# Performance work log

Measured on AMD Instinct MI355X. Metric: run time of the kernel, lower is better.

The kernel has to match this reference:

```python
import jax, jax.numpy as jnp
import numpy as np

N_NODES = 100000
N_EDGES = 1600000
N_GRAPHS = 2048
IN_C, HID, OUT_C, EDGE_DIM = 32, 128, 1, 3


def _glorot(key, shape):
    fan_in, fan_out = shape[0], shape[1]
    lim = np.sqrt(6.0 / (fan_in + fan_out))
    return jax.random.uniform(key, shape, jnp.float32, -lim, lim)


def setup_inputs() -> dict:
    key = jax.random.key(0)
    ks = jax.random.split(key, 16)
    x = jax.random.normal(ks[0], (N_NODES, IN_C), jnp.float32)
    edge_index = jax.random.randint(ks[1], (2, N_EDGES), 0, N_NODES, jnp.int64)
    edge_attr = jax.random.uniform(ks[2], (N_EDGES, EDGE_DIM), jnp.float32)
    batch = jnp.sort(jax.random.randint(ks[3], (N_NODES,), 0, N_GRAPHS, jnp.int64))
    params = {
        # GINEConv 1: edge lin 3->32, nn1: 32->128->128
        "We1": _glorot(ks[4], (EDGE_DIM, IN_C)), "be1": jnp.zeros((IN_C,), jnp.float32),
        "W1a": _glorot(ks[5], (IN_C, HID)), "b1a": jnp.zeros((HID,), jnp.float32),
        "W1b": _glorot(ks[6], (HID, HID)), "b1b": jnp.zeros((HID,), jnp.float32),
        # GINEConv 2: edge lin 3->128, nn2: 128->128->128
        "We2": _glorot(ks[7], (EDGE_DIM, HID)), "be2": jnp.zeros((HID,), jnp.float32),
        "W2a": _glorot(ks[8], (HID, HID)), "b2a": jnp.zeros((HID,), jnp.float32),
        "W2b": _glorot(ks[9], (HID, HID)), "b2b": jnp.zeros((HID,), jnp.float32),
        # readout MLP: 128->128->1
        "Wm1": _glorot(ks[10], (HID, HID)), "bm1": jnp.zeros((HID,), jnp.float32),
        "Wm2": _glorot(ks[11], (HID, OUT_C)), "bm2": jnp.zeros((OUT_C,), jnp.float32),
    }
    return {"x": x, "edge_index": edge_index, "edge_attr": edge_attr, "batch": batch, **params}


def _gine_conv(x, src, dst, edge_attr, We, be, Wa, ba, Wb, bb):
    # message: relu(x_j + lin(edge_attr)); aggregate: scatter-add at dst; eps=0
    msg = jax.nn.relu(x[src] + edge_attr @ We + be)          # [E, C]
    agg = jax.ops.segment_sum(msg, dst, num_segments=x.shape[0])
    h = x + agg                                              # (1+eps)*x + agg, eps=0
    return jax.nn.relu(h @ Wa + ba) @ Wb + bb


def reference(x, edge_index, edge_attr, batch,
              We1, be1, W1a, b1a, W1b, b1b,
              We2, be2, W2a, b2a, W2b, b2b,
              Wm1, bm1, Wm2, bm2):
    src, dst = edge_index[0], edge_index[1]
    h = jax.nn.relu(_gine_conv(x, src, dst, edge_attr, We1, be1, W1a, b1a, W1b, b1b))
    h = jax.nn.relu(_gine_conv(h, src, dst, edge_attr, We2, be2, W2a, b2a, W2b, b2b))
    pooled = jax.ops.segment_sum(h, batch, num_segments=N_GRAPHS)  # global_add_pool
    return jax.nn.relu(pooled @ Wm1 + bm1) @ Wm2 + bm2
```

## Files before the change

### kernel.cpp

```cpp
#include <hip/hip_runtime.h>
#include <hip/hip_bf16.h>

#define NN 100000
#define NE 1600000
#define NG 2048
#define NBKT 196
#define EPB 4096
#define BINBLKS ((NE + EPB - 1) / EPB)

typedef __attribute__((ext_vector_type(8))) short short8v;
typedef __attribute__((ext_vector_type(4))) float f32x4;

__device__ inline ushort f2bf(float f) {
    uint u = __float_as_uint(f);
    uint r = (u + 0x7fffu + ((u >> 16) & 1u)) >> 16;
    return (ushort)r;
}
__device__ inline float bf2f(ushort h) {
    return __uint_as_float(((uint)h) << 16);
}

#define MFMA_BF16 __builtin_amdgcn_mfma_f32_16x16x32_bf16

__device__ inline int frag128(int k, int c) {
    int w = c >> 5, half = (c >> 4) & 1, cl = c & 15;
    int ksl = k >> 5, kq = (k >> 3) & 3, k0 = k & 7;
    return ((ksl * 4 + w) * 2 + half) * 512 + (kq * 16 + cl) * 8 + k0;
}
__device__ inline int frag32(int k, int c) {
    int w = c >> 5, half = (c >> 4) & 1, cl = c & 15;
    int kq = (k >> 3) & 3, k0 = k & 7;
    return (w * 2 + half) * 512 + (kq * 16 + cl) * 8 + k0;
}


__global__ __launch_bounds__(256) void k_bhist(const int* __restrict__ dst,
                                               int* __restrict__ bhist) {
    __shared__ int h[NBKT];
    int t = threadIdx.x;
    for (int i = t; i < NBKT; i += 256) h[i] = 0;
    __syncthreads();
    int e0 = blockIdx.x * EPB;
    int n = NE - e0; if (n > EPB) n = EPB;
    for (int i = t; i < n; i += 256)
        atomicAdd(&h[dst[e0 + i] >> 9], 1);
    __syncthreads();
    for (int i = t; i < NBKT; i += 256)
        if (h[i]) atomicAdd(&bhist[i], h[i]);
}

__global__ void k_bscan(const int* __restrict__ bhist,
                        int* __restrict__ bkt_off, int* __restrict__ bkt_cursor) {
    __shared__ int s[256];
    int t = threadIdx.x;
    int v = (t < NBKT) ? bhist[t] : 0;
    s[t] = v;
    __syncthreads();
    for (int off = 1; off < 256; off <<= 1) {
        int add = (t >= off) ? s[t - off] : 0;
        __syncthreads();
        s[t] += add;
        __syncthreads();
    }
    int excl = s[t] - v;
    if (t < NBKT) { bkt_off[t] = excl; bkt_cursor[t] = excl; }
    if (t == NBKT - 1) bkt_off[NBKT] = excl + v;
}


__global__ __launch_bounds__(256) void k_binfill(
        const int* __restrict__ src, const int* __restrict__ dst,
        const float* __restrict__ ea,
        int* __restrict__ bkt_cursor, uint2* __restrict__ tmp) {
    __shared__ int hist[NBKT];
    __shared__ int boff[NBKT];
    __shared__ int base[NBKT];
    __shared__ int s[256];
    __shared__ uint2 stage[EPB];
    __shared__ unsigned char stage_bkt[EPB];
    int t = threadIdx.x;
    int e0 = blockIdx.x * EPB;
    int n = NE - e0; if (n > EPB) n = EPB;

    for (int i = t; i < NBKT; i += 256) hist[i] = 0;
    __syncthreads();

    uint lo[16], hi[16]; int bk[16], pos[16];
#pragma unroll
    for (int j = 0; j < 16; ++j) {
        int i = j * 256 + t;
        bk[j] = -1;
        if (i < n) {
            int e = e0 + i;
            int sn = src[e], d = dst[e];
            uint q0 = (uint)__float2int_rn(ea[3 * e]     * 1023.f);
            uint q1 = (uint)__float2int_rn(ea[3 * e + 1] * 1023.f);
            uint q2 = (uint)__float2int_rn(ea[3 * e + 2] * 1023.f);
            uint q = (q0 << 20) | (q1 << 10) | q2;
            lo[j] = (uint)sn | ((uint)(d & 0x7FFF) << 17);
            hi[j] = (uint)(d >> 15) | (q << 2);
            bk[j] = d >> 9;
            pos[j] = atomicAdd(&hist[bk[j]], 1);
        }
    }
    __syncthreads();
    int v = (t < NBKT) ? hist[t] : 0;
    s[t] = v;
    __syncthreads();
    for (int off = 1; off < 256; off <<= 1) {
        int add = (t >= off) ? s[t - off] : 0;
        __syncthreads();
        s[t] += add;
        __syncthreads();
    }
    if (t < NBKT) {
        boff[t] = s[t] - v;
        base[t] = v ? atomicAdd(&bkt_cursor[t], v) : 0;
    }
    __syncthreads();
#pragma unroll
    for (int j = 0; j < 16; ++j) {
        if (bk[j] >= 0) {
            int slot = boff[bk[j]] + pos[j];
            stage[slot] = make_uint2(lo[j], hi[j]);
            stage_bkt[slot] = (unsigned char)bk[j];
        }
    }
    __syncthreads();
    for (int i = t; i < n; i += 256) {
        int b = stage_bkt[i];
        tmp[base[b] + (i - boff[b])] = stage[i];
    }
}


__global__ __launch_bounds__(256) void k_scatter(
        const uint2* __restrict__ tmp, const int* __restrict__ bkt_off,
        int* __restrict__ row_ptr, uint2* __restrict__ csr) {
    __shared__ int hist[512];
    __shared__ int cur[512];
    __shared__ int s[256];
    int b = blockIdx.x, t = threadIdx.x;
    int start = bkt_off[b], end = bkt_off[b + 1];
    hist[t] = 0; hist[t + 256] = 0;
    __syncthreads();
    for (int i = start + t; i < end; i += 256) {
        uint2 r = tmp[i];
        int d = (int)((r.x >> 17) | ((r.y & 3u) << 15));
        atomicAdd(&hist[d & 511], 1);
    }
    __syncthreads();
    int h0 = hist[2 * t], h1 = hist[2 * t + 1];
    int v = h0 + h1;
    s[t] = v;
    __syncthreads();
    for (int off = 1; off < 256; off <<= 1) {
        int add = (t >= off) ? s[t - off] : 0;
        __syncthreads();
        s[t] += add;
        __syncthreads();
    }
    int e0 = start + s[t] - v;
    int node0 = b * 512 + 2 * t;
    if (node0 < NN) row_ptr[node0] = e0;
    if (node0 + 1 < NN) row_ptr[node0 + 1] = e0 + h0;
    cur[2 * t] = e0;
    cur[2 * t + 1] = e0 + h0;
    if (b == NBKT - 1 && t == 0) row_ptr[NN] = end;
    __syncthreads();
    for (int i = start + t; i < end; i += 256) {
        uint2 r = tmp[i];
        int sn = (int)(r.x & 0x1FFFFu);
        int d = (int)((r.x >> 17) | ((r.y & 3u) << 15));
        int p = atomicAdd(&cur[d & 511], 1);
        csr[p] = make_uint2((uint)sn, r.y >> 2);
    }
}


__global__ void k_xcast(const float* __restrict__ x, ushort* __restrict__ xb) {
    int i = blockIdx.x * 256 + threadIdx.x;
    if (i < NN * 32 / 4) {
        float4 v = ((const float4*)x)[i];
        ushort4 o;
        o.x = f2bf(v.x); o.y = f2bf(v.y); o.z = f2bf(v.z); o.w = f2bf(v.w);
        ((ushort4*)xb)[i] = o;
    }
}


__global__ void k_prep(const float* __restrict__ W1a, const float* __restrict__ W1b,
                       const float* __restrict__ W2a, const float* __restrict__ W2b,
                       ushort* __restrict__ W1a_hi, ushort* __restrict__ W1a_lo,
                       ushort* __restrict__ W1b_hi, ushort* __restrict__ W1b_lo,
                       ushort* __restrict__ W2a_hi, ushort* __restrict__ W2a_lo,
                       ushort* __restrict__ W2b_hi, ushort* __restrict__ W2b_lo) {
    int i = blockIdx.x * 256 + threadIdx.x;
    float v; ushort* ph; ushort* pl; int off;
    if (i < 4096) {
        int k = i >> 7, c = i & 127;
        v = W1a[i]; ph = W1a_hi; pl = W1a_lo; off = frag32(k, c);
    } else if (i < 20480) {
        int j = i - 4096; int k = j >> 7, c = j & 127;
        v = W1b[j]; ph = W1b_hi; pl = W1b_lo; off = frag128(k, c);
    } else if (i < 36864) {
        int j = i - 20480; int k = j >> 7, c = j & 127;
        v = W2a[j]; ph = W2a_hi; pl = W2a_lo; off = frag128(k, c);
    } else if (i < 53248) {
        int j = i - 36864; int k = j >> 7, c = j & 127;
        v = W2b[j]; ph = W2b_hi; pl = W2b_lo; off = frag128(k, c);
    } else return;
    ushort h = f2bf(v);
    ph[off] = h;
    pl[off] = f2bf(v - bf2f(h));
}


__global__ __launch_bounds__(256) void k_agg1(
        const ushort* __restrict__ xb, const uint2* __restrict__ csr,
        const int* __restrict__ row_ptr,
        const float* __restrict__ We1, const float* __restrict__ be1,
        float* __restrict__ agg1) {
    int lane = threadIdx.x & 31;
    int node = blockIdx.x * 8 + (threadIdx.x >> 5);
    const float qs = 1.f / 1023.f;
    float w0 = We1[lane] * qs, w1 = We1[32 + lane] * qs, w2 = We1[64 + lane] * qs;
    float b = be1[lane];
    int p0 = row_ptr[node], p1 = row_ptr[node + 1];
    float acc = 0.f;
    int p = p0;
    for (; p + 8 <= p1; p += 8) {
        uint2 e[8]; ushort v[8];
#pragma unroll
        for (int j = 0; j < 8; ++j) e[j] = csr[p + j];
#pragma unroll
        for (int j = 0; j < 8; ++j) v[j] = xb[e[j].x * 32 + lane];
#pragma unroll
        for (int j = 0; j < 8; ++j) {
            float a0 = (float)(e[j].y >> 20);
            float a1 = (float)((e[j].y >> 10) & 1023u);
            float a2 = (float)(e[j].y & 1023u);
            float el = fmaf(a0, w0, fmaf(a1, w1, fmaf(a2, w2, b)));
            acc += fmaxf(bf2f(v[j]) + el, 0.f);
        }
    }
    for (; p + 4 <= p1; p += 4) {
        uint2 e[4]; ushort v[4];
#pragma unroll
        for (int j = 0; j < 4; ++j) e[j] = csr[p + j];
#pragma unroll
        for (int j = 0; j < 4; ++j) v[j] = xb[e[j].x * 32 + lane];
#pragma unroll
        for (int j = 0; j < 4; ++j) {
            float a0 = (float)(e[j].y >> 20);
            float a1 = (float)((e[j].y >> 10) & 1023u);
            float a2 = (float)(e[j].y & 1023u);
            float el = fmaf(a0, w0, fmaf(a1, w1, fmaf(a2, w2, b)));
            acc += fmaxf(bf2f(v[j]) + el, 0.f);
        }
    }
    for (; p < p1; ++p) {
        uint2 ed = csr[p];
        ushort v = xb[ed.x * 32 + lane];
        float a0 = (float)(ed.y >> 20);
        float a1 = (float)((ed.y >> 10) & 1023u);
        float a2 = (float)(ed.y & 1023u);
        float el = fmaf(a0, w0, fmaf(a1, w1, fmaf(a2, w2, b)));
        acc += fmaxf(bf2f(v) + el, 0.f);
    }
    agg1[node * 32 + lane] = acc;
}


__global__ __launch_bounds__(256) void k_agg2(
        const ushort* __restrict__ h1b, const uint2* __restrict__ csr,
        const int* __restrict__ row_ptr,
        const float* __restrict__ We2, const float* __restrict__ be2,
        float* __restrict__ agg2) {
    int lane = threadIdx.x & 63;
    int node = __builtin_amdgcn_readfirstlane(blockIdx.x * 4 + (threadIdx.x >> 6));
    int c = lane * 2;
    const float qs = 1.f / 1023.f;
    float w0a = We2[c] * qs,       w0b = We2[c + 1] * qs;
    float w1a = We2[128 + c] * qs, w1b = We2[129 + c] * qs;
    float w2a = We2[256 + c] * qs, w2b = We2[257 + c] * qs;
    float ba  = be2[c],            bb  = be2[c + 1];
    const uint* h1u = (const uint*)h1b;
    int p0 = __builtin_amdgcn_readfirstlane(row_ptr[node]);
    int p1 = __builtin_amdgcn_readfirstlane(row_ptr[node + 1]);
    float accA = 0.f, accB = 0.f;
    int p = p0;
    for (; p + 8 <= p1; p += 8) {
        uint2 e[8]; uint u[8];
#pragma unroll
        for (int j = 0; j < 8; ++j) e[j] = csr[p + j];
#pragma unroll
        for (int j = 0; j < 8; ++j) u[j] = h1u[e[j].x * 64 + lane];
#pragma unroll
        for (int j = 0; j < 8; ++j) {
            float a0 = (float)(e[j].y >> 20);
            float a1 = (float)((e[j].y >> 10) & 1023u);
            float a2 = (float)(e[j].y & 1023u);
            float elA = fmaf(a0, w0a, fmaf(a1, w1a, fmaf(a2, w2a, ba)));
            float elB = fmaf(a0, w0b, fmaf(a1, w1b, fmaf(a2, w2b, bb)));
            accA += fmaxf(bf2f((ushort)(u[j] & 0xffffu)) + elA, 0.f);
            accB += fmaxf(bf2f((ushort)(u[j] >> 16)) + elB, 0.f);
        }
    }
    for (; p + 4 <= p1; p += 4) {
        uint2 e[4]; uint u[4];
#pragma unroll
        for (int j = 0; j < 4; ++j) e[j] = csr[p + j];
#pragma unroll
        for (int j = 0; j < 4; ++j) u[j] = h1u[e[j].x * 64 + lane];
#pragma unroll
        for (int j = 0; j < 4; ++j) {
            float a0 = (float)(e[j].y >> 20);
            float a1 = (float)((e[j].y >> 10) & 1023u);
            float a2 = (float)(e[j].y & 1023u);
            float elA = fmaf(a0, w0a, fmaf(a1, w1a, fmaf(a2, w2a, ba)));
            float elB = fmaf(a0, w0b, fmaf(a1, w1b, fmaf(a2, w2b, bb)));
            accA += fmaxf(bf2f((ushort)(u[j] & 0xffffu)) + elA, 0.f);
            accB += fmaxf(bf2f((ushort)(u[j] >> 16)) + elB, 0.f);
        }
    }
    for (; p < p1; ++p) {
        uint2 ed = csr[p];
        uint u = h1u[ed.x * 64 + lane];
        float a0 = (float)(ed.y >> 20);
        float a1 = (float)((ed.y >> 10) & 1023u);
        float a2 = (float)(ed.y & 1023u);
        float elA = fmaf(a0, w0a, fmaf(a1, w1a, fmaf(a2, w2a, ba)));
        float elB = fmaf(a0, w0b, fmaf(a1, w1b, fmaf(a2, w2b, bb)));
        accA += fmaxf(bf2f((ushort)(u & 0xffffu)) + elA, 0.f);
        accB += fmaxf(bf2f((ushort)(u >> 16)) + elB, 0.f);
    }
    *(float2*)&agg2[node * 128 + c] = make_float2(accA, accB);
}


#define M1_AHI 0
#define M1_ALO 2560
#define M1_HHI 5120
#define M1_HLO 13824
#define M1_SMEM 22528

__global__ __launch_bounds__(256) void k_mlp1(
        const float* __restrict__ x, const float* __restrict__ agg1,
        const ushort* __restrict__ W1a_hi, const ushort* __restrict__ W1a_lo,
        const float* __restrict__ b1a,
        const ushort* __restrict__ W1b_hi, const ushort* __restrict__ W1b_lo,
        const float* __restrict__ b1b,
        ushort* __restrict__ h1b) {
    __shared__ __align__(16) char smem[M1_SMEM];
    ushort* A_hi = (ushort*)(smem + M1_AHI);
    ushort* A_lo = (ushort*)(smem + M1_ALO);
    ushort* H_hi = (ushort*)(smem + M1_HHI);
    ushort* H_lo = (ushort*)(smem + M1_HLO);
    int t = threadIdx.x;
    int nbase = blockIdx.x * 32;

    if (t < 128) {
        int n = t >> 2, cc = (t & 3) * 8;
        int gn = nbase + n;
        short8v vh = {0,0,0,0,0,0,0,0}, vl = {0,0,0,0,0,0,0,0};
        if (gn < NN) {
            const float4* xp = (const float4*)&x[gn * 32 + cc];
            const float4* gp = (const float4*)&agg1[gn * 32 + cc];
            float s[8];
            float4 x0 = xp[0], x1 = xp[1], g0 = gp[0], g1 = gp[1];
            s[0]=x0.x+g0.x; s[1]=x0.y+g0.y; s[2]=x0.z+g0.z; s[3]=x0.w+g0.w;
            s[4]=x1.x+g1.x; s[5]=x1.y+g1.y; s[6]=x1.z+g1.z; s[7]=x1.w+g1.w;
#pragma unroll
            for (int j = 0; j < 8; ++j) {
                ushort h = f2bf(s[j]);
                vh[j] = (short)h;
                vl[j] = (short)f2bf(s[j] - bf2f(h));
            }
        }
        *(short8v*)&A_hi[n * 40 + cc] = vh;
        *(short8v*)&A_lo[n * 40 + cc] = vl;
    }
    __syncthreads();

    int w = t >> 6, l = t & 63;
    int cl = l & 15, kq = l >> 4;
    int row0 = w * 32 + cl, row1 = w * 32 + 16 + cl;

    f32x4 acc[2][2];
#pragma unroll
    for (int mt = 0; mt < 2; ++mt) { acc[mt][0] = f32x4{0.f,0.f,0.f,0.f}; acc[mt][1] = f32x4{0.f,0.f,0.f,0.f}; }

    {
        int kof = kq * 8;
        int fb = (w * 2) * 512 + l * 8;
        short8v bh0 = *(const short8v*)&W1a_hi[fb];
        short8v bh1 = *(const short8v*)&W1a_hi[fb + 512];
        short8v bl0 = *(const short8v*)&W1a_lo[fb];
        short8v bl1 = *(const short8v*)&W1a_lo[fb + 512];
#pragma unroll
        for (int mt = 0; mt < 2; ++mt) {
            short8v ah = *(short8v*)&A_hi[(mt * 16 + cl) * 40 + kof];
            short8v al = *(short8v*)&A_lo[(mt * 16 + cl) * 40 + kof];
            acc[mt][0] = MFMA_BF16(ah, bh0, acc[mt][0], 0, 0, 0);
            acc[mt][0] = MFMA_BF16(al, bh0, acc[mt][0], 0, 0, 0);
            acc[mt][0] = MFMA_BF16(ah, bl0, acc[mt][0], 0, 0, 0);
            acc[mt][1] = MFMA_BF16(ah, bh1, acc[mt][1], 0, 0, 0);
            acc[mt][1] = MFMA_BF16(al, bh1, acc[mt][1], 0, 0, 0);
            acc[mt][1] = MFMA_BF16(ah, bl1, acc[mt][1], 0, 0, 0);
        }
    }
    {
        float bb0 = b1a[row0], bb1 = b1a[row1];
#pragma unroll
        for (int mt = 0; mt < 2; ++mt)
#pragma unroll
            for (int j = 0; j < 4; ++j) {
                int row = mt * 16 + kq * 4 + j;
                float v0 = fmaxf(acc[mt][0][j] + bb0, 0.f);
                float v1 = fmaxf(acc[mt][1][j] + bb1, 0.f);
                ushort h0 = f2bf(v0), h1v = f2bf(v1);
                H_hi[row * 136 + row0] = h0;
                H_lo[row * 136 + row0] = f2bf(v0 - bf2f(h0));
                H_hi[row * 136 + row1] = h1v;
                H_lo[row * 136 + row1] = f2bf(v1 - bf2f(h1v));
            }
    }
    __syncthreads();

#pragma unroll
    for (int mt = 0; mt < 2; ++mt) { acc[mt][0] = f32x4{0.f,0.f,0.f,0.f}; acc[mt][1] = f32x4{0.f,0.f,0.f,0.f}; }
#pragma unroll
    for (int ksl = 0; ksl < 4; ++ksl) {
        int kof = ksl * 32 + kq * 8;
        int fb = ((ksl * 4 + w) * 2) * 512 + l * 8;
        short8v bh0 = *(const short8v*)&W1b_hi[fb];
        short8v bh1 = *(const short8v*)&W1b_hi[fb + 512];
        short8v bl0 = *(const short8v*)&W1b_lo[fb];
        short8v bl1 = *(const short8v*)&W1b_lo[fb + 512];
#pragma unroll
        for (int mt = 0; mt < 2; ++mt) {
            short8v ah = *(short8v*)&H_hi[(mt * 16 + cl) * 136 + kof];
            short8v al = *(short8v*)&H_lo[(mt * 16 + cl) * 136 + kof];
            acc[mt][0] = MFMA_BF16(ah, bh0, acc[mt][0], 0, 0, 0);
            acc[mt][0] = MFMA_BF16(al, bh0, acc[mt][0], 0, 0, 0);
            acc[mt][0] = MFMA_BF16(ah, bl0, acc[mt][0], 0, 0, 0);
            acc[mt][1] = MFMA_BF16(ah, bh1, acc[mt][1], 0, 0, 0);
            acc[mt][1] = MFMA_BF16(al, bh1, acc[mt][1], 0, 0, 0);
            acc[mt][1] = MFMA_BF16(ah, bl1, acc[mt][1], 0, 0, 0);
        }
    }
    {
        float c0 = b1b[row0], c1 = b1b[row1];
#pragma unroll
        for (int mt = 0; mt < 2; ++mt)
#pragma unroll
            for (int j = 0; j < 4; ++j) {
                int gn = nbase + mt * 16 + kq * 4 + j;
                if (gn < NN) {
                    h1b[gn * 128 + row0] = f2bf(fmaxf(acc[mt][0][j] + c0, 0.f));
                    h1b[gn * 128 + row1] = f2bf(fmaxf(acc[mt][1][j] + c1, 0.f));
                }
            }
    }
}


#define M2_AHI 0
#define M2_ALO 8704
#define M2_HHI 17408
#define M2_HLO 26112
#define M2_B   34816
#define M2_SMEM 34944

__global__ __launch_bounds__(256) void k_mlp2(
        const ushort* __restrict__ h1b, const float* __restrict__ agg2,
        const ushort* __restrict__ W2a_hi, const ushort* __restrict__ W2a_lo,
        const float* __restrict__ b2a,
        const ushort* __restrict__ W2b_hi, const ushort* __restrict__ W2b_lo,
        const float* __restrict__ b2b,
        const int* __restrict__ batch, float* __restrict__ pooled) {
    __shared__ __align__(16) char smem[M2_SMEM];
    ushort* A_hi = (ushort*)(smem + M2_AHI);
    ushort* A_lo = (ushort*)(smem + M2_ALO);
    ushort* H_hi = (ushort*)(smem + M2_HHI);
    ushort* H_lo = (ushort*)(smem + M2_HLO);
    int* batch_s = (int*)(smem + M2_B);
    int t = threadIdx.x;
    int nbase = blockIdx.x * 32;

    if (t < 32) batch_s[t] = (nbase + t < NN) ? batch[nbase + t] : -1;

    for (int i = t; i < 512; i += 256) {
        int n = i >> 4, cc = (i & 15) * 8;
        int gn = nbase + n;
        short8v vh = {0,0,0,0,0,0,0,0}, vl = {0,0,0,0,0,0,0,0};
        if (gn < NN) {
            short8v hb = *(const short8v*)&h1b[gn * 128 + cc];
            const float4* gp = (const float4*)&agg2[gn * 128 + cc];
            float4 g0 = gp[0], g1 = gp[1];
            float s[8];
            s[0]=bf2f((ushort)hb[0])+g0.x; s[1]=bf2f((ushort)hb[1])+g0.y;
            s[2]=bf2f((ushort)hb[2])+g0.z; s[3]=bf2f((ushort)hb[3])+g0.w;
            s[4]=bf2f((ushort)hb[4])+g1.x; s[5]=bf2f((ushort)hb[5])+g1.y;
            s[6]=bf2f((ushort)hb[6])+g1.z; s[7]=bf2f((ushort)hb[7])+g1.w;
#pragma unroll
            for (int j = 0; j < 8; ++j) {
                ushort h = f2bf(s[j]);
                vh[j] = (short)h;
                vl[j] = (short)f2bf(s[j] - bf2f(h));
            }
        }
        *(short8v*)&A_hi[n * 136 + cc] = vh;
        *(short8v*)&A_lo[n * 136 + cc] = vl;
    }
    __syncthreads();

    int w = t >> 6, l = t & 63;
    int cl = l & 15, kq = l >> 4;
    int row0 = w * 32 + cl, row1 = w * 32 + 16 + cl;

    f32x4 acc[2][2];
#pragma unroll
    for (int mt = 0; mt < 2; ++mt) { acc[mt][0] = f32x4{0.f,0.f,0.f,0.f}; acc[mt][1] = f32x4{0.f,0.f,0.f,0.f}; }

#pragma unroll
    for (int ksl = 0; ksl < 4; ++ksl) {
        int kof = ksl * 32 + kq * 8;
        int fb = ((ksl * 4 + w) * 2) * 512 + l * 8;
        short8v bh0 = *(const short8v*)&W2a_hi[fb];
        short8v bh1 = *(const short8v*)&W2a_hi[fb + 512];
        short8v bl0 = *(const short8v*)&W2a_lo[fb];
        short8v bl1 = *(const short8v*)&W2a_lo[fb + 512];
#pragma unroll
        for (int mt = 0; mt < 2; ++mt) {
            short8v ah = *(short8v*)&A_hi[(mt * 16 + cl) * 136 + kof];
            short8v al = *(short8v*)&A_lo[(mt * 16 + cl) * 136 + kof];
            acc[mt][0] = MFMA_BF16(ah, bh0, acc[mt][0], 0, 0, 0);
            acc[mt][0] = MFMA_BF16(al, bh0, acc[mt][0], 0, 0, 0);
            acc[mt][0] = MFMA_BF16(ah, bl0, acc[mt][0], 0, 0, 0);
            acc[mt][1] = MFMA_BF16(ah, bh1, acc[mt][1], 0, 0, 0);
            acc[mt][1] = MFMA_BF16(al, bh1, acc[mt][1], 0, 0, 0);
            acc[mt][1] = MFMA_BF16(ah, bl1, acc[mt][1], 0, 0, 0);
        }
    }
    {
        float bb0 = b2a[row0], bb1 = b2a[row1];
#pragma unroll
        for (int mt = 0; mt < 2; ++mt)
#pragma unroll
            for (int j = 0; j < 4; ++j) {
                int row = mt * 16 + kq * 4 + j;
                float v0 = fmaxf(acc[mt][0][j] + bb0, 0.f);
                float v1 = fmaxf(acc[mt][1][j] + bb1, 0.f);
                ushort h0 = f2bf(v0), h1v = f2bf(v1);
                H_hi[row * 136 + row0] = h0;
                H_lo[row * 136 + row0] = f2bf(v0 - bf2f(h0));
                H_hi[row * 136 + row1] = h1v;
                H_lo[row * 136 + row1] = f2bf(v1 - bf2f(h1v));
            }
    }
    __syncthreads();

#pragma unroll
    for (int mt = 0; mt < 2; ++mt) { acc[mt][0] = f32x4{0.f,0.f,0.f,0.f}; acc[mt][1] = f32x4{0.f,0.f,0.f,0.f}; }
#pragma unroll
    for (int ksl = 0; ksl < 4; ++ksl) {
        int kof = ksl * 32 + kq * 8;
        int fb = ((ksl * 4 + w) * 2) * 512 + l * 8;
        short8v bh0 = *(const short8v*)&W2b_hi[fb];
        short8v bh1 = *(const short8v*)&W2b_hi[fb + 512];
        short8v bl0 = *(const short8v*)&W2b_lo[fb];
        short8v bl1 = *(const short8v*)&W2b_lo[fb + 512];
#pragma unroll
        for (int mt = 0; mt < 2; ++mt) {
            short8v ah = *(short8v*)&H_hi[(mt * 16 + cl) * 136 + kof];
            short8v al = *(short8v*)&H_lo[(mt * 16 + cl) * 136 + kof];
            acc[mt][0] = MFMA_BF16(ah, bh0, acc[mt][0], 0, 0, 0);
            acc[mt][0] = MFMA_BF16(al, bh0, acc[mt][0], 0, 0, 0);
            acc[mt][0] = MFMA_BF16(ah, bl0, acc[mt][0], 0, 0, 0);
            acc[mt][1] = MFMA_BF16(ah, bh1, acc[mt][1], 0, 0, 0);
            acc[mt][1] = MFMA_BF16(al, bh1, acc[mt][1], 0, 0, 0);
            acc[mt][1] = MFMA_BF16(ah, bl1, acc[mt][1], 0, 0, 0);
        }
    }
    __syncthreads();
    float* P = (float*)smem;
    {
        float c0 = b2b[row0], c1 = b2b[row1];
#pragma unroll
        for (int mt = 0; mt < 2; ++mt)
#pragma unroll
            for (int j = 0; j < 4; ++j) {
                int row = mt * 16 + kq * 4 + j;
                P[row * 132 + row0] = fmaxf(acc[mt][0][j] + c0, 0.f);
                P[row * 132 + row1] = fmaxf(acc[mt][1][j] + c1, 0.f);
            }
    }
    __syncthreads();

    {
        int c = t & 127, half = t >> 7;
        int i0 = half * 16;
        float run = 0.f;
        int cur = batch_s[i0];
        if (cur >= 0) {
            for (int i = i0; i < i0 + 16; ++i) {
                int b = batch_s[i];
                if (b < 0) break;
                if (b != cur) { atomicAdd(&pooled[cur * 128 + c], run); run = 0.f; cur = b; }
                run += P[i * 132 + c];
            }
            atomicAdd(&pooled[cur * 128 + c], run);
        }
    }
}


__global__ __launch_bounds__(128) void k_readout(
        const float* __restrict__ pooled, const float* __restrict__ Wm1,
        const float* __restrict__ bm1, const float* __restrict__ Wm2,
        const float* __restrict__ bm2, float* __restrict__ out) {
    __shared__ float row[128];
    __shared__ float red[128];
    int g = blockIdx.x, t = threadIdx.x;
    row[t] = pooled[g * 128 + t];
    __syncthreads();
    float acc = bm1[t];
    for (int c = 0; c < 128; ++c) acc = fmaf(row[c], Wm1[c * 128 + t], acc);
    float term = fmaxf(acc, 0.f) * Wm2[t];
    red[t] = term;
    __syncthreads();
    for (int off = 64; off > 0; off >>= 1) {
        if (t < off) red[t] += red[t + off];
        __syncthreads();
    }
    if (t == 0) out[g] = red[0] + bm2[0];
}


extern "C" void kernel_launch(void* const* d_in, const int* in_sizes, int n_in,
                              void* d_out, int out_size, void* d_ws, size_t ws_size,
                              hipStream_t stream) {
    const float* x    = (const float*)d_in[0];
    const int* eidx   = (const int*)d_in[1];
    const float* ea   = (const float*)d_in[2];
    const int* batch  = (const int*)d_in[3];
    const float* We1  = (const float*)d_in[4];
    const float* be1  = (const float*)d_in[5];
    const float* W1a  = (const float*)d_in[6];
    const float* b1a  = (const float*)d_in[7];
    const float* W1b  = (const float*)d_in[8];
    const float* b1b  = (const float*)d_in[9];
    const float* We2  = (const float*)d_in[10];
    const float* be2  = (const float*)d_in[11];
    const float* W2a  = (const float*)d_in[12];
    const float* b2a  = (const float*)d_in[13];
    const float* W2b  = (const float*)d_in[14];
    const float* b2b  = (const float*)d_in[15];
    const float* Wm1  = (const float*)d_in[16];
    const float* bm1  = (const float*)d_in[17];
    const float* Wm2  = (const float*)d_in[18];
    const float* bm2  = (const float*)d_in[19];
    float* out = (float*)d_out;

    const int* src = eidx;
    const int* dst = eidx + NE;

    char* w = (char*)d_ws;
    auto alloc = [&](size_t bytes) { void* p = (void*)w; w += (bytes + 255) & ~(size_t)255; return p; };
    int* row_ptr    = (int*)alloc((NN + 1) * 4);
    int* bhist      = (int*)alloc(256 * 4);
    int* bkt_off    = (int*)alloc(256 * 4);
    int* bkt_cursor = (int*)alloc(256 * 4);
    uint2* csr      = (uint2*)alloc((size_t)NE * 8);
    uint2* tmp      = (uint2*)alloc((size_t)NE * 8);
    float* agg1     = (float*)alloc((size_t)NN * 32 * 4);
    ushort* h1b     = (ushort*)alloc((size_t)NN * 128 * 2);
    float* agg2     = (float*)alloc((size_t)NN * 128 * 4);
    float* pooled   = (float*)alloc((size_t)NG * 128 * 4);
    ushort* xb      = (ushort*)alloc((size_t)NN * 32 * 2);
    ushort* W1a_hi  = (ushort*)alloc(4096 * 2);
    ushort* W1a_lo  = (ushort*)alloc(4096 * 2);
    ushort* W1b_hi  = (ushort*)alloc(16384 * 2);
    ushort* W1b_lo  = (ushort*)alloc(16384 * 2);
    ushort* W2a_hi  = (ushort*)alloc(16384 * 2);
    ushort* W2a_lo  = (ushort*)alloc(16384 * 2);
    ushort* W2b_hi  = (ushort*)alloc(16384 * 2);
    ushort* W2b_lo  = (ushort*)alloc(16384 * 2);

    hipMemsetAsync(bhist, 0, 256 * 4, stream);
    hipMemsetAsync(pooled, 0, (size_t)NG * 128 * 4, stream);

    const int MB = (NN + 31) / 32;

    k_prep<<<208, 256, 0, stream>>>(W1a, W1b, W2a, W2b,
                                    W1a_hi, W1a_lo, W1b_hi, W1b_lo,
                                    W2a_hi, W2a_lo, W2b_hi, W2b_lo);
    k_xcast<<<3125, 256, 0, stream>>>(x, xb);
    k_bhist<<<BINBLKS, 256, 0, stream>>>(dst, bhist);
    k_bscan<<<1, 256, 0, stream>>>(bhist, bkt_off, bkt_cursor);
    k_binfill<<<BINBLKS, 256, 0, stream>>>(src, dst, ea, bkt_cursor, tmp);
    k_scatter<<<NBKT, 256, 0, stream>>>(tmp, bkt_off, row_ptr, csr);

    k_agg1<<<NN / 8, 256, 0, stream>>>(xb, csr, row_ptr, We1, be1, agg1);
    k_mlp1<<<MB, 256, 0, stream>>>(x, agg1, W1a_hi, W1a_lo, b1a, W1b_hi, W1b_lo, b1b, h1b);
    k_agg2<<<NN / 4, 256, 0, stream>>>(h1b, csr, row_ptr, We2, be2, agg2);
    k_mlp2<<<MB, 256, 0, stream>>>(h1b, agg2, W2a_hi, W2a_lo, b2a, W2b_hi, W2b_lo, b2b, batch, pooled);
    k_readout<<<NG, 128, 0, stream>>>(pooled, Wm1, bm1, Wm2, bm2, out);
}
```

Baseline: 335.3 us.

## Fuse layer-2 edge aggregation into the MLP2 kernel, dropping the agg2 buffer

The separate k_agg2 kernel is removed. Each wavefront of k_mlp2 now gathers and aggregates the incoming edge messages for 8 nodes directly into the shared-memory A tile before the MFMA stage. This avoids writing and re-reading the fp32 agg2 array (about 51 MB) and drops one kernel launch. In exchange, the gather now runs in blocks of 32 nodes with 8 serial nodes per wave, giving fewer waves for latency hiding. The NN bound checks were also removed, which is safe only because NN is a multiple of 32.

```diff
diff --git a/kernel.cpp b/kernel.cpp
--- a/kernel.cpp
+++ b/kernel.cpp
@@ -272,73 +272,6 @@
 }
 
 
-__global__ __launch_bounds__(256) void k_agg2(
-        const ushort* __restrict__ h1b, const uint2* __restrict__ csr,
-        const int* __restrict__ row_ptr,
-        const float* __restrict__ We2, const float* __restrict__ be2,
-        float* __restrict__ agg2) {
-    int lane = threadIdx.x & 63;
-    int node = __builtin_amdgcn_readfirstlane(blockIdx.x * 4 + (threadIdx.x >> 6));
-    int c = lane * 2;
-    const float qs = 1.f / 1023.f;
-    float w0a = We2[c] * qs,       w0b = We2[c + 1] * qs;
-    float w1a = We2[128 + c] * qs, w1b = We2[129 + c] * qs;
-    float w2a = We2[256 + c] * qs, w2b = We2[257 + c] * qs;
-    float ba  = be2[c],            bb  = be2[c + 1];
-    const uint* h1u = (const uint*)h1b;
-    int p0 = __builtin_amdgcn_readfirstlane(row_ptr[node]);
-    int p1 = __builtin_amdgcn_readfirstlane(row_ptr[node + 1]);
-    float accA = 0.f, accB = 0.f;
-    int p = p0;
-    for (; p + 8 <= p1; p += 8) {
-        uint2 e[8]; uint u[8];
-#pragma unroll
-        for (int j = 0; j < 8; ++j) e[j] = csr[p + j];
-#pragma unroll
-        for (int j = 0; j < 8; ++j) u[j] = h1u[e[j].x * 64 + lane];
-#pragma unroll
-        for (int j = 0; j < 8; ++j) {
-            float a0 = (float)(e[j].y >> 20);
-            float a1 = (float)((e[j].y >> 10) & 1023u);
-            float a2 = (float)(e[j].y & 1023u);
-            float elA = fmaf(a0, w0a, fmaf(a1, w1a, fmaf(a2, w2a, ba)));
-            float elB = fmaf(a0, w0b, fmaf(a1, w1b, fmaf(a2, w2b, bb)));
-            accA += fmaxf(bf2f((ushort)(u[j] & 0xffffu)) + elA, 0.f);
-            accB += fmaxf(bf2f((ushort)(u[j] >> 16)) + elB, 0.f);
-        }
-    }
-    for (; p + 4 <= p1; p += 4) {
-        uint2 e[4]; uint u[4];
-#pragma unroll
-        for (int j = 0; j < 4; ++j) e[j] = csr[p + j];
-#pragma unroll
-        for (int j = 0; j < 4; ++j) u[j] = h1u[e[j].x * 64 + lane];
-#pragma unroll
-        for (int j = 0; j < 4; ++j) {
-            float a0 = (float)(e[j].y >> 20);
-            float a1 = (float)((e[j].y >> 10) & 1023u);
-            float a2 = (float)(e[j].y & 1023u);
-            float elA = fmaf(a0, w0a, fmaf(a1, w1a, fmaf(a2, w2a, ba)));
-            float elB = fmaf(a0, w0b, fmaf(a1, w1b, fmaf(a2, w2b, bb)));
-            accA += fmaxf(bf2f((ushort)(u[j] & 0xffffu)) + elA, 0.f);
-            accB += fmaxf(bf2f((ushort)(u[j] >> 16)) + elB, 0.f);
-        }
-    }
-    for (; p < p1; ++p) {
-        uint2 ed = csr[p];
-        uint u = h1u[ed.x * 64 + lane];
-        float a0 = (float)(ed.y >> 20);
-        float a1 = (float)((ed.y >> 10) & 1023u);
-        float a2 = (float)(ed.y & 1023u);
-        float elA = fmaf(a0, w0a, fmaf(a1, w1a, fmaf(a2, w2a, ba)));
-        float elB = fmaf(a0, w0b, fmaf(a1, w1b, fmaf(a2, w2b, bb)));
-        accA += fmaxf(bf2f((ushort)(u & 0xffffu)) + elA, 0.f);
-        accB += fmaxf(bf2f((ushort)(u >> 16)) + elB, 0.f);
-    }
-    *(float2*)&agg2[node * 128 + c] = make_float2(accA, accB);
-}
-
-
 #define M1_AHI 0
 #define M1_ALO 2560
 #define M1_HHI 5120
@@ -474,7 +407,9 @@
 #define M2_SMEM 34944
 
 __global__ __launch_bounds__(256) void k_mlp2(
-        const ushort* __restrict__ h1b, const float* __restrict__ agg2,
+        const ushort* __restrict__ h1b, const uint2* __restrict__ csr,
+        const int* __restrict__ row_ptr,
+        const float* __restrict__ We2, const float* __restrict__ be2,
         const ushort* __restrict__ W2a_hi, const ushort* __restrict__ W2a_lo,
         const float* __restrict__ b2a,
         const ushort* __restrict__ W2b_hi, const ushort* __restrict__ W2b_lo,
@@ -487,36 +422,82 @@
     ushort* H_lo = (ushort*)(smem + M2_HLO);
     int* batch_s = (int*)(smem + M2_B);
     int t = threadIdx.x;
+    int w = t >> 6, l = t & 63;
     int nbase = blockIdx.x * 32;
 
-    if (t < 32) batch_s[t] = (nbase + t < NN) ? batch[nbase + t] : -1;
-
-    for (int i = t; i < 512; i += 256) {
-        int n = i >> 4, cc = (i & 15) * 8;
-        int gn = nbase + n;
-        short8v vh = {0,0,0,0,0,0,0,0}, vl = {0,0,0,0,0,0,0,0};
-        if (gn < NN) {
-            short8v hb = *(const short8v*)&h1b[gn * 128 + cc];
-            const float4* gp = (const float4*)&agg2[gn * 128 + cc];
-            float4 g0 = gp[0], g1 = gp[1];
-            float s[8];
-            s[0]=bf2f((ushort)hb[0])+g0.x; s[1]=bf2f((ushort)hb[1])+g0.y;
-            s[2]=bf2f((ushort)hb[2])+g0.z; s[3]=bf2f((ushort)hb[3])+g0.w;
-            s[4]=bf2f((ushort)hb[4])+g1.x; s[5]=bf2f((ushort)hb[5])+g1.y;
-            s[6]=bf2f((ushort)hb[6])+g1.z; s[7]=bf2f((ushort)hb[7])+g1.w;
-#pragma unroll
-            for (int j = 0; j < 8; ++j) {
-                ushort h = f2bf(s[j]);
-                vh[j] = (short)h;
-                vl[j] = (short)f2bf(s[j] - bf2f(h));
-            }
-        }
-        *(short8v*)&A_hi[n * 136 + cc] = vh;
-        *(short8v*)&A_lo[n * 136 + cc] = vl;
-    }
-    __syncthreads();
-
-    int w = t >> 6, l = t & 63;
+    if (t < 32) batch_s[t] = batch[nbase + t];
+
+    {
+        int c = l * 2;
+        const float qs = 1.f / 1023.f;
+        float w0a = We2[c] * qs,       w0b = We2[c + 1] * qs;
+        float w1a = We2[128 + c] * qs, w1b = We2[129 + c] * qs;
+        float w2a = We2[256 + c] * qs, w2b = We2[257 + c] * qs;
+        float ba  = be2[c],            bb  = be2[c + 1];
+        const uint* h1u = (const uint*)h1b;
+        for (int i = 0; i < 8; ++i) {
+            int nn = nbase + w * 8 + i;
+            int p0 = __builtin_amdgcn_readfirstlane(row_ptr[nn]);
+            int p1 = __builtin_amdgcn_readfirstlane(row_ptr[nn + 1]);
+            float accA = 0.f, accB = 0.f;
+            int p = p0;
+            for (; p + 8 <= p1; p += 8) {
+                uint2 e[8]; uint u[8];
+#pragma unroll
+                for (int j = 0; j < 8; ++j) e[j] = csr[p + j];
+#pragma unroll
+                for (int j = 0; j < 8; ++j) u[j] = h1u[e[j].x * 64 + l];
+#pragma unroll
+                for (int j = 0; j < 8; ++j) {
+                    float a0 = (float)(e[j].y >> 20);
+                    float a1 = (float)((e[j].y >> 10) & 1023u);
+                    float a2 = (float)(e[j].y & 1023u);
+                    float elA = fmaf(a0, w0a, fmaf(a1, w1a, fmaf(a2, w2a, ba)));
+                    float elB = fmaf(a0, w0b, fmaf(a1, w1b, fmaf(a2, w2b, bb)));
+                    accA += fmaxf(bf2f((ushort)(u[j] & 0xffffu)) + elA, 0.f);
+                    accB += fmaxf(bf2f((ushort)(u[j] >> 16)) + elB, 0.f);
+                }
+            }
+            for (; p + 4 <= p1; p += 4) {
+                uint2 e[4]; uint u[4];
+#pragma unroll
+                for (int j = 0; j < 4; ++j) e[j] = csr[p + j];
+#pragma unroll
+                for (int j = 0; j < 4; ++j) u[j] = h1u[e[j].x * 64 + l];
+#pragma unroll
+                for (int j = 0; j < 4; ++j) {
+                    float a0 = (float)(e[j].y >> 20);
+                    float a1 = (float)((e[j].y >> 10) & 1023u);
+                    float a2 = (float)(e[j].y & 1023u);
+                    float elA = fmaf(a0, w0a, fmaf(a1, w1a, fmaf(a2, w2a, ba)));
+                    float elB = fmaf(a0, w0b, fmaf(a1, w1b, fmaf(a2, w2b, bb)));
+                    accA += fmaxf(bf2f((ushort)(u[j] & 0xffffu)) + elA, 0.f);
+                    accB += fmaxf(bf2f((ushort)(u[j] >> 16)) + elB, 0.f);
+                }
+            }
+            for (; p < p1; ++p) {
+                uint2 ed = csr[p];
+                uint u = h1u[ed.x * 64 + l];
+                float a0 = (float)(ed.y >> 20);
+                float a1 = (float)((ed.y >> 10) & 1023u);
+                float a2 = (float)(ed.y & 1023u);
+                float elA = fmaf(a0, w0a, fmaf(a1, w1a, fmaf(a2, w2a, ba)));
+                float elB = fmaf(a0, w0b, fmaf(a1, w1b, fmaf(a2, w2b, bb)));
+                accA += fmaxf(bf2f((ushort)(u & 0xffffu)) + elA, 0.f);
+                accB += fmaxf(bf2f((ushort)(u >> 16)) + elB, 0.f);
+            }
+            uint u = h1u[nn * 64 + l];
+            float sA = bf2f((ushort)(u & 0xffffu)) + accA;
+            float sB = bf2f((ushort)(u >> 16)) + accB;
+            ushort hA = f2bf(sA), hB = f2bf(sB);
+            ushort lA = f2bf(sA - bf2f(hA)), lB = f2bf(sB - bf2f(hB));
+            int n = w * 8 + i;
+            *(uint*)&A_hi[n * 136 + c] = (uint)hA | ((uint)hB << 16);
+            *(uint*)&A_lo[n * 136 + c] = (uint)lA | ((uint)lB << 16);
+        }
+    }
+    __syncthreads();
+
     int cl = l & 15, kq = l >> 4;
     int row0 = w * 32 + cl, row1 = w * 32 + 16 + cl;
 
@@ -604,15 +585,12 @@
         int i0 = half * 16;
         float run = 0.f;
         int cur = batch_s[i0];
-        if (cur >= 0) {
-            for (int i = i0; i < i0 + 16; ++i) {
-                int b = batch_s[i];
-                if (b < 0) break;
-                if (b != cur) { atomicAdd(&pooled[cur * 128 + c], run); run = 0.f; cur = b; }
-                run += P[i * 132 + c];
-            }
-            atomicAdd(&pooled[cur * 128 + c], run);
-        }
+        for (int i = i0; i < i0 + 16; ++i) {
+            int b = batch_s[i];
+            if (b != cur) { atomicAdd(&pooled[cur * 128 + c], run); run = 0.f; cur = b; }
+            run += P[i * 132 + c];
+        }
+        atomicAdd(&pooled[cur * 128 + c], run);
     }
 }
 
@@ -677,7 +655,6 @@
     uint2* tmp      = (uint2*)alloc((size_t)NE * 8);
     float* agg1     = (float*)alloc((size_t)NN * 32 * 4);
     ushort* h1b     = (ushort*)alloc((size_t)NN * 128 * 2);
-    float* agg2     = (float*)alloc((size_t)NN * 128 * 4);
     float* pooled   = (float*)alloc((size_t)NG * 128 * 4);
     ushort* xb      = (ushort*)alloc((size_t)NN * 32 * 2);
     ushort* W1a_hi  = (ushort*)alloc(4096 * 2);
@@ -705,7 +682,7 @@
 
     k_agg1<<<NN / 8, 256, 0, stream>>>(xb, csr, row_ptr, We1, be1, agg1);
     k_mlp1<<<MB, 256, 0, stream>>>(x, agg1, W1a_hi, W1a_lo, b1a, W1b_hi, W1b_lo, b1b, h1b);
-    k_agg2<<<NN / 4, 256, 0, stream>>>(h1b, csr, row_ptr, We2, be2, agg2);
-    k_mlp2<<<MB, 256, 0, stream>>>(h1b, agg2, W2a_hi, W2a_lo, b2a, W2b_hi, W2b_lo, b2b, batch, pooled);
+    k_mlp2<<<MB, 256, 0, stream>>>(h1b, csr, row_ptr, We2, be2,
+                                   W2a_hi, W2a_lo, b2a, W2b_hi, W2b_lo, b2b, batch, pooled);
     k_readout<<<NG, 128, 0, stream>>>(pooled, Wm1, bm1, Wm2, bm2, out);
 }
```

Result: slower. 354.1 us (+5.6%).
